# Optimization experiments

Measured on AMD Instinct MI355X. Metric: run time of the kernel, lower is better.

Reference implementation:

```python
import jax, jax.numpy as jnp
import numpy as np


def setup_inputs() -> dict:
    key = jax.random.key(0)
    k1, k2, k3 = jax.random.split(key, 3)
    B, gd, gh, gw = 4, 8, 16, 16
    H, W = 1024, 1024
    grid = jax.random.normal(k1, (B, 12, gd, gh, gw), dtype=jnp.float32)
    guide = jax.random.uniform(k2, (B, H, W), dtype=jnp.float32)
    image = jax.random.uniform(k3, (B, 3, H, W), dtype=jnp.float32)
    return {"grid": grid, "guide": guide, "image": image}


def _slice_apply(grid, guide, image):
    # grid: [B, 12, gd, gh, gw]; guide: [B, H, W] in [0,1]; image: [B, 3, H, W]
    B, C, gd, gh, gw = grid.shape
    _, h, w = guide.shape
    dt = grid.dtype
    # continuous grid coordinates (Halide reference convention)
    gx = (jnp.arange(w, dtype=dt) + 0.5) * gw / w          # [w]
    gy = (jnp.arange(h, dtype=dt) + 0.5) * gh / h          # [h]
    gz = guide * gd                                        # [B,h,w]
    fx = jnp.floor(gx - 0.5)
    fy = jnp.floor(gy - 0.5)
    fz = jnp.floor(gz - 0.5)
    bidx = jnp.arange(B)[:, None, None]
    coeffs = jnp.zeros((B, h, w, C), dt)
    # 8-corner trilinear gather with tent weights (clamped borders)
    for dz in (0, 1):
        zf = fz + dz
        wz = jnp.maximum(1.0 - jnp.abs(zf + 0.5 - gz), 0.0)       # [B,h,w]
        iz = jnp.clip(zf, 0, gd - 1).astype(jnp.int32)
        for dy in (0, 1):
            yf = fy + dy
            wy = jnp.maximum(1.0 - jnp.abs(yf + 0.5 - gy), 0.0)   # [h]
            iy = jnp.clip(yf, 0, gh - 1).astype(jnp.int32)
            for dx in (0, 1):
                xf = fx + dx
                wx = jnp.maximum(1.0 - jnp.abs(xf + 0.5 - gx), 0.0)  # [w]
                ix = jnp.clip(xf, 0, gw - 1).astype(jnp.int32)
                # gather -> [B,h,w,C]
                g = grid[bidx, :, iz, iy[None, :, None], ix[None, None, :]]
                wgt = wz * wy[None, :, None] * wx[None, None, :]
                coeffs = coeffs + g * wgt[..., None]
    # per-pixel 3x4 affine transform: out_i = sum_j A_ij * in_j + b_i
    co = coeffs.reshape(B, h, w, 3, 4)
    out = jnp.einsum('bhwij,bjhw->bihw', co[..., :3], image) + co[..., 3].transpose(0, 3, 1, 2)
    return out


def reference(grid, guide, image):
    return _slice_apply(grid, guide, image)
```

## Files before the change

kernel.cpp:

```cpp
#include <hip/hip_runtime.h>

#define IMH 1024
#define IMW 1024
#define GD 8
#define GH 16
#define GW 16
#define NC 12

__global__ __launch_bounds__(256) void bsa_kernel(
    const float* __restrict__ grid,
    const float* __restrict__ guide,
    const float* __restrict__ image,
    float* __restrict__ out)
{
    const int y = blockIdx.x;
    const int b = blockIdx.y;

    __shared__ __align__(16) float sG[GW][GD][NC];

    const float gy  = (y + 0.5f) * ((float)GH / IMH);
    const float fyf = floorf(gy - 0.5f);
    const float ty  = gy - 0.5f - fyf;
    const int   fy  = (int)fyf;
    const int   iy0 = min(GH - 1, max(0, fy));
    const int   iy1 = min(GH - 1, max(0, fy + 1));

    const float* gb = grid + (size_t)b * NC * GD * GH * GW;
    for (int i = threadIdx.x; i < GD * GW * NC; i += 256) {
        const int x = i & (GW - 1);
        const int z = (i >> 4) & (GD - 1);
        const int c = i >> 7;
        const float v0 = gb[((c * GD + z) * GH + iy0) * GW + x];
        const float v1 = gb[((c * GD + z) * GH + iy1) * GW + x];
        sG[x][z][c] = v0 + ty * (v1 - v0);
    }
    __syncthreads();

    const size_t plane = (size_t)IMH * IMW;
    const float* gp = guide + ((size_t)b * IMH + y) * IMW;
    const float* ip = image + ((size_t)b * 3 * IMH + y) * IMW;
    float*       op = out   + ((size_t)b * 3 * IMH + y) * IMW;

#pragma unroll
    for (int p = 0; p < 4; ++p) {
        const int x = threadIdx.x + 256 * p;

        const float gv = gp[x];
        const float rv = ip[x];
        const float g2 = ip[x + plane];
        const float bv = ip[x + 2 * plane];

        const float gx  = (x + 0.5f) * ((float)GW / IMW);
        const float fxf = floorf(gx - 0.5f);
        const float tx  = gx - 0.5f - fxf;
        const int   fx  = (int)fxf;
        const int   ix0 = min(GW - 1, max(0, fx));
        const int   ix1 = min(GW - 1, max(0, fx + 1));

        const float gz  = gv * (float)GD;
        const float fzf = floorf(gz - 0.5f);
        const float tz  = gz - 0.5f - fzf;
        const int   fzi = (int)fzf;
        const int   iz0 = min(GD - 1, max(0, fzi));
        const int   iz1 = min(GD - 1, max(0, fzi + 1));

        const float w00 = (1.0f - tz) * (1.0f - tx);
        const float w01 = (1.0f - tz) * tx;
        const float w10 = tz * (1.0f - tx);
        const float w11 = tz * tx;

        const float* p00 = &sG[ix0][iz0][0];
        const float* p01 = &sG[ix1][iz0][0];
        const float* p10 = &sG[ix0][iz1][0];
        const float* p11 = &sG[ix1][iz1][0];

        float res[3];
#pragma unroll
        for (int i = 0; i < 3; ++i) {
            const float4 a = *(const float4*)(p00 + 4 * i);
            const float4 c = *(const float4*)(p01 + 4 * i);
            const float4 d = *(const float4*)(p10 + 4 * i);
            const float4 e = *(const float4*)(p11 + 4 * i);
            const float c0 = w00 * a.x + w01 * c.x + w10 * d.x + w11 * e.x;
            const float c1 = w00 * a.y + w01 * c.y + w10 * d.y + w11 * e.y;
            const float c2 = w00 * a.z + w01 * c.z + w10 * d.z + w11 * e.z;
            const float c3 = w00 * a.w + w01 * c.w + w10 * d.w + w11 * e.w;
            res[i] = c0 * rv + c1 * g2 + c2 * bv + c3;
        }

        op[x]             = res[0];
        op[x + plane]     = res[1];
        op[x + 2 * plane] = res[2];
    }
}

extern "C" void kernel_launch(void* const* d_in, const int* in_sizes, int n_in,
                              void* d_out, int out_size, void* d_ws, size_t ws_size,
                              hipStream_t stream) {
    const float* grid  = (const float*)d_in[0];
    const float* guide = (const float*)d_in[1];
    const float* image = (const float*)d_in[2];
    float* out = (float*)d_out;

    const int B = in_sizes[1] / (IMH * IMW);
    dim3 g(IMH, B);
    bsa_kernel<<<g, 256, 0, stream>>>(grid, guide, image, out);
}
```

Baseline: 118.8 us.

## Process four rows per block with double-buffered shared grid slice prefetch

Each block now handles four image rows instead of one, so the grid is a quarter of its former size and the per-column x-weights are computed once and reused across rows. The y-interpolated grid slice for the next row is loaded into registers while the current row is processed, then written to a second shared buffer, with one barrier per row. The aim is to amortize the per-block slice setup and hide grid-load latency. The cost is more registers, fewer blocks, and extra barriers.

```diff
diff --git a/kernel.cpp b/kernel.cpp
--- a/kernel.cpp
+++ b/kernel.cpp
@@ -6,6 +6,7 @@
 #define GH 16
 #define GW 16
 #define NC 12
+#define ROWS 4
 
 __global__ __launch_bounds__(256) void bsa_kernel(
     const float* __restrict__ grid,
@@ -13,84 +14,136 @@
     const float* __restrict__ image,
     float* __restrict__ out)
 {
-    const int y = blockIdx.x;
-    const int b = blockIdx.y;
+    const int y0  = blockIdx.x * ROWS;
+    const int b   = blockIdx.y;
+    const int tid = threadIdx.x;
 
-    __shared__ __align__(16) float sG[GW][GD][NC];
-
-    const float gy  = (y + 0.5f) * ((float)GH / IMH);
-    const float fyf = floorf(gy - 0.5f);
-    const float ty  = gy - 0.5f - fyf;
-    const int   fy  = (int)fyf;
-    const int   iy0 = min(GH - 1, max(0, fy));
-    const int   iy1 = min(GH - 1, max(0, fy + 1));
+    __shared__ __align__(16) float sG[2][GW][GD][NC];
+    float* const sbase_ptr = &sG[0][0][0][0];
+    const int SBUF = GW * GD * NC;
 
     const float* gb = grid + (size_t)b * NC * GD * GH * GW;
-    for (int i = threadIdx.x; i < GD * GW * NC; i += 256) {
+
+    int gsrc[6];
+    int soff[6];
+    #pragma unroll
+    for (int k = 0; k < 6; ++k) {
+        const int i = tid + 256 * k;
         const int x = i & (GW - 1);
         const int z = (i >> 4) & (GD - 1);
         const int c = i >> 7;
-        const float v0 = gb[((c * GD + z) * GH + iy0) * GW + x];
-        const float v1 = gb[((c * GD + z) * GH + iy1) * GW + x];
-        sG[x][z][c] = v0 + ty * (v1 - v0);
+        gsrc[k] = ((c * GD + z) * GH) * GW + x;
+        soff[k] = (x * GD + z) * NC + c;
+    }
+
+    int   ix0v[4], ix1v[4];
+    float txv[4];
+    #pragma unroll
+    for (int p = 0; p < 4; ++p) {
+        const int   x   = tid + 256 * p;
+        const float gx  = (x + 0.5f) * ((float)GW / IMW);
+        const float fxf = floorf(gx - 0.5f);
+        txv[p]  = gx - 0.5f - fxf;
+        const int fx = (int)fxf;
+        ix0v[p] = min(GW - 1, max(0, fx));
+        ix1v[p] = min(GW - 1, max(0, fx + 1));
+    }
+
+    {
+        const float gy  = (y0 + 0.5f) * ((float)GH / IMH);
+        const float fyf = floorf(gy - 0.5f);
+        const float ty  = gy - 0.5f - fyf;
+        const int   fy  = (int)fyf;
+        const int   iy0 = min(GH - 1, max(0, fy));
+        const int   iy1 = min(GH - 1, max(0, fy + 1));
+        #pragma unroll
+        for (int k = 0; k < 6; ++k) {
+            const float v0 = gb[gsrc[k] + iy0 * GW];
+            const float v1 = gb[gsrc[k] + iy1 * GW];
+            sbase_ptr[soff[k]] = v0 + ty * (v1 - v0);
+        }
     }
     __syncthreads();
 
     const size_t plane = (size_t)IMH * IMW;
-    const float* gp = guide + ((size_t)b * IMH + y) * IMW;
-    const float* ip = image + ((size_t)b * 3 * IMH + y) * IMW;
-    float*       op = out   + ((size_t)b * 3 * IMH + y) * IMW;
 
-#pragma unroll
-    for (int p = 0; p < 4; ++p) {
-        const int x = threadIdx.x + 256 * p;
-
-        const float gv = gp[x];
-        const float rv = ip[x];
-        const float g2 = ip[x + plane];
-        const float bv = ip[x + 2 * plane];
-
-        const float gx  = (x + 0.5f) * ((float)GW / IMW);
-        const float fxf = floorf(gx - 0.5f);
-        const float tx  = gx - 0.5f - fxf;
-        const int   fx  = (int)fxf;
-        const int   ix0 = min(GW - 1, max(0, fx));
-        const int   ix1 = min(GW - 1, max(0, fx + 1));
-
-        const float gz  = gv * (float)GD;
-        const float fzf = floorf(gz - 0.5f);
-        const float tz  = gz - 0.5f - fzf;
-        const int   fzi = (int)fzf;
-        const int   iz0 = min(GD - 1, max(0, fzi));
-        const int   iz1 = min(GD - 1, max(0, fzi + 1));
-
-        const float w00 = (1.0f - tz) * (1.0f - tx);
-        const float w01 = (1.0f - tz) * tx;
-        const float w10 = tz * (1.0f - tx);
-        const float w11 = tz * tx;
-
-        const float* p00 = &sG[ix0][iz0][0];
-        const float* p01 = &sG[ix1][iz0][0];
-        const float* p10 = &sG[ix0][iz1][0];
-        const float* p11 = &sG[ix1][iz1][0];
-
-        float res[3];
-#pragma unroll
-        for (int i = 0; i < 3; ++i) {
-            const float4 a = *(const float4*)(p00 + 4 * i);
-            const float4 c = *(const float4*)(p01 + 4 * i);
-            const float4 d = *(const float4*)(p10 + 4 * i);
-            const float4 e = *(const float4*)(p11 + 4 * i);
-            const float c0 = w00 * a.x + w01 * c.x + w10 * d.x + w11 * e.x;
-            const float c1 = w00 * a.y + w01 * c.y + w10 * d.y + w11 * e.y;
-            const float c2 = w00 * a.z + w01 * c.z + w10 * d.z + w11 * e.z;
-            const float c3 = w00 * a.w + w01 * c.w + w10 * d.w + w11 * e.w;
-            res[i] = c0 * rv + c1 * g2 + c2 * bv + c3;
+    #pragma unroll
+    for (int j = 0; j < ROWS; ++j) {
+        float nv0[6], nv1[6], nty = 0.0f;
+        if (j + 1 < ROWS) {
+            const int   yn  = y0 + j + 1;
+            const float gy  = (yn + 0.5f) * ((float)GH / IMH);
+            const float fyf = floorf(gy - 0.5f);
+            nty = gy - 0.5f - fyf;
+            const int fy  = (int)fyf;
+            const int iy0 = min(GH - 1, max(0, fy));
+            const int iy1 = min(GH - 1, max(0, fy + 1));
+            #pragma unroll
+            for (int k = 0; k < 6; ++k) {
+                nv0[k] = gb[gsrc[k] + iy0 * GW];
+                nv1[k] = gb[gsrc[k] + iy1 * GW];
+            }
         }
 
-        op[x]             = res[0];
-        op[x + plane]     = res[1];
-        op[x + 2 * plane] = res[2];
+        const int y = y0 + j;
+        const float* gp = guide + ((size_t)b * IMH + y) * IMW;
+        const float* ip = image + ((size_t)b * 3 * IMH + y) * IMW;
+        float*       op = out   + ((size_t)b * 3 * IMH + y) * IMW;
+        const float* S  = sbase_ptr + (j & 1) * SBUF;
+
+        #pragma unroll
+        for (int p = 0; p < 4; ++p) {
+            const int x = tid + 256 * p;
+
+            const float gv = gp[x];
+            const float rv = ip[x];
+            const float g2 = ip[x + plane];
+            const float bv = ip[x + 2 * plane];
+
+            const float gz  = gv * (float)GD;
+            const float fzf = floorf(gz - 0.5f);
+            const float tz  = gz - 0.5f - fzf;
+            const int   fzi = (int)fzf;
+            const int   iz0 = min(GD - 1, max(0, fzi));
+            const int   iz1 = min(GD - 1, max(0, fzi + 1));
+
+            const float tx  = txv[p];
+            const float w00 = (1.0f - tz) * (1.0f - tx);
+            const float w01 = (1.0f - tz) * tx;
+            const float w10 = tz * (1.0f - tx);
+            const float w11 = tz * tx;
+
+            const float* p00 = S + (ix0v[p] * GD + iz0) * NC;
+            const float* p01 = S + (ix1v[p] * GD + iz0) * NC;
+            const float* p10 = S + (ix0v[p] * GD + iz1) * NC;
+            const float* p11 = S + (ix1v[p] * GD + iz1) * NC;
+
+            float res[3];
+            #pragma unroll
+            for (int i = 0; i < 3; ++i) {
+                const float4 a = *(const float4*)(p00 + 4 * i);
+                const float4 c = *(const float4*)(p01 + 4 * i);
+                const float4 d = *(const float4*)(p10 + 4 * i);
+                const float4 e = *(const float4*)(p11 + 4 * i);
+                const float c0 = w00 * a.x + w01 * c.x + w10 * d.x + w11 * e.x;
+                const float c1 = w00 * a.y + w01 * c.y + w10 * d.y + w11 * e.y;
+                const float c2 = w00 * a.z + w01 * c.z + w10 * d.z + w11 * e.z;
+                const float c3 = w00 * a.w + w01 * c.w + w10 * d.w + w11 * e.w;
+                res[i] = c0 * rv + c1 * g2 + c2 * bv + c3;
+            }
+
+            op[x]             = res[0];
+            op[x + plane]     = res[1];
+            op[x + 2 * plane] = res[2];
+        }
+
+        if (j + 1 < ROWS) {
+            float* D = sbase_ptr + ((j + 1) & 1) * SBUF;
+            #pragma unroll
+            for (int k = 0; k < 6; ++k)
+                D[soff[k]] = nv0[k] + nty * (nv1[k] - nv0[k]);
+        }
+        __syncthreads();
     }
 }
 
@@ -103,6 +156,6 @@
     float* out = (float*)d_out;
 
     const int B = in_sizes[1] / (IMH * IMW);
-    dim3 g(IMH, B);
+    dim3 g(IMH / ROWS, B);
     bsa_kernel<<<g, 256, 0, stream>>>(grid, guide, image, out);
 }
```

New measurement: 119.0 us. Within noise of the previous version (+0.1%).
